# Optimization experiments

Measured on AMD Instinct MI355X. Metric: run time of the kernel, lower is better.

Reference implementation:

```python
import jax, jax.numpy as jnp
import numpy as np

B, H, W, C = 32, 112, 112, 128
R = 2048  # make_divisible(128*16, 8)

def setup_inputs() -> dict:
    key = jax.random.key(0)
    k1, k2, k3 = jax.random.split(key, 3)
    x = jax.random.normal(k1, (B, H, W, C), dtype=jnp.float32)
    w1 = jax.random.normal(k2, (C, R), dtype=jnp.float32) * (1.0 / np.sqrt(C))
    b1 = jnp.zeros((R,), dtype=jnp.float32)
    w2 = jax.random.normal(k3, (R, C), dtype=jnp.float32) * (1.0 / np.sqrt(R))
    b2 = jnp.zeros((C,), dtype=jnp.float32)
    return {"x": x, "w1": w1, "b1": b1, "w2": w2, "b2": b2}

def reference(x, w1, b1, w2, b2):
    # squeeze: global average pool over H, W -> [B, C]
    s = jnp.mean(x, axis=(1, 2))
    # excite: two 1x1 convs on pooled vector == matmuls
    h = jax.nn.gelu(s @ w1 + b1)          # [B, R], tanh-approx GELU (tfa default)
    g = jax.nn.sigmoid(h @ w2 + b2)       # [B, C]
    # broadcast gate over spatial dims
    return x * g[:, None, None, :]
```

## Files before the change

### kernel.cpp

```cpp
#include <hip/hip_runtime.h>
#include <math.h>

#define B_ 32
#define H_ 112
#define W_ 112
#define C_ 128
#define R_ 2048
#define HW_ (H_ * W_)
#define C4_ (C_ / 4)
#define PB_ 32
#define RB_ 8

typedef float f32x4_t __attribute__((ext_vector_type(4)));

__global__ __launch_bounds__(256) void pool_kernel(const float4* __restrict__ x,
                                                   float4* __restrict__ part) {
    const int b     = blockIdx.x;
    const int pb    = blockIdx.y;
    const int t     = threadIdx.x;
    const int lane4 = t & 31;
    const int prow  = t >> 5;

    const int pixels_per_block = HW_ / PB_;
    const int p0 = pb * pixels_per_block;
    const float4* xb = x + (size_t)b * HW_ * C4_;

    float4 acc = make_float4(0.f, 0.f, 0.f, 0.f);
    for (int p = p0 + prow; p < p0 + pixels_per_block; p += 8) {
        float4 v = xb[(size_t)p * C4_ + lane4];
        acc.x += v.x; acc.y += v.y; acc.z += v.z; acc.w += v.w;
    }

    __shared__ float4 red[256];
    red[t] = acc;
    __syncthreads();
    if (t < 32) {
        float4 a = red[t];
#pragma unroll
        for (int k = 1; k < 8; ++k) {
            float4 v = red[t + 32 * k];
            a.x += v.x; a.y += v.y; a.z += v.z; a.w += v.w;
        }
        part[((size_t)b * PB_ + pb) * C4_ + t] = a;
    }
}

__global__ __launch_bounds__(256) void fc_kernel(const float4* __restrict__ part,
                                                 const float* __restrict__ w1,
                                                 const float* __restrict__ b1,
                                                 const float4* __restrict__ w2,
                                                 float4* __restrict__ gpart) {
    const int b  = blockIdx.x >> 3;
    const int rb = blockIdx.x & 7;
    const int t  = threadIdx.x;
    const int r  = rb * 256 + t;

    __shared__ float  sl[C_];
    __shared__ float  hl[256];
    __shared__ float4 red[256];

    if (t < 32) {
        float4 a = make_float4(0.f, 0.f, 0.f, 0.f);
#pragma unroll 8
        for (int k = 0; k < PB_; ++k) {
            float4 v = part[((size_t)b * PB_ + k) * C4_ + t];
            a.x += v.x; a.y += v.y; a.z += v.z; a.w += v.w;
        }
        const float inv = 1.0f / (float)HW_;
        sl[t * 4 + 0] = a.x * inv;
        sl[t * 4 + 1] = a.y * inv;
        sl[t * 4 + 2] = a.z * inv;
        sl[t * 4 + 3] = a.w * inv;
    }
    __syncthreads();

    float acc = b1[r];
#pragma unroll 8
    for (int c = 0; c < C_; ++c)
        acc += sl[c] * w1[(size_t)c * R_ + r];

    const float xv = acc;
    const float tn = tanhf(0.7978845608028654f * (xv + 0.044715f * xv * xv * xv));
    hl[t] = 0.5f * xv * (1.0f + tn);
    __syncthreads();

    const int c4 = t & 31;
    const int ks = t >> 5;
    float4 a2 = make_float4(0.f, 0.f, 0.f, 0.f);
    const int rr0 = ks * 32;
#pragma unroll 8
    for (int rr = rr0; rr < rr0 + 32; ++rr) {
        const float hv = hl[rr];
        float4 w = w2[(size_t)(rb * 256 + rr) * C4_ + c4];
        a2.x += hv * w.x; a2.y += hv * w.y; a2.z += hv * w.z; a2.w += hv * w.w;
    }
    red[t] = a2;
    __syncthreads();
    if (t < 32) {
        float4 a = red[t];
#pragma unroll
        for (int k = 1; k < 8; ++k) {
            float4 v = red[t + 32 * k];
            a.x += v.x; a.y += v.y; a.z += v.z; a.w += v.w;
        }
        gpart[((size_t)b * RB_ + rb) * C4_ + t] = a;
    }
}

__global__ __launch_bounds__(256) void scale_kernel(const float4* __restrict__ x,
                                                    const float4* __restrict__ gpart,
                                                    const float* __restrict__ b2,
                                                    float4* __restrict__ out) {
    const int b  = blockIdx.x;
    const int t  = threadIdx.x;
    const int c4 = t & 31;

    const float4* gp = gpart + (size_t)b * RB_ * C4_;
    float4 a = gp[c4];
#pragma unroll
    for (int k = 1; k < RB_; ++k) {
        float4 v = gp[(size_t)k * C4_ + c4];
        a.x += v.x; a.y += v.y; a.z += v.z; a.w += v.w;
    }
    a.x += b2[c4 * 4 + 0]; a.y += b2[c4 * 4 + 1];
    a.z += b2[c4 * 4 + 2]; a.w += b2[c4 * 4 + 3];
    float4 gv;
    gv.x = 1.0f / (1.0f + expf(-a.x));
    gv.y = 1.0f / (1.0f + expf(-a.y));
    gv.z = 1.0f / (1.0f + expf(-a.z));
    gv.w = 1.0f / (1.0f + expf(-a.w));

    const size_t base = (size_t)b * HW_ * C4_;
    const int total = HW_ * C4_;
    const int stride = gridDim.y * 256;

    for (int i = blockIdx.y * 256 + t; i < total; i += stride) {
        float4 v = x[base + i];
        f32x4_t o;
        o.x = v.x * gv.x; o.y = v.y * gv.y; o.z = v.z * gv.z; o.w = v.w * gv.w;
        __builtin_nontemporal_store(o, (f32x4_t*)&out[base + i]);
    }
}

extern "C" void kernel_launch(void* const* d_in, const int* in_sizes, int n_in,
                              void* d_out, int out_size, void* d_ws, size_t ws_size,
                              hipStream_t stream) {
    const float* x  = (const float*)d_in[0];
    const float* w1 = (const float*)d_in[1];
    const float* b1 = (const float*)d_in[2];
    const float* w2 = (const float*)d_in[3];
    const float* b2 = (const float*)d_in[4];
    float* out = (float*)d_out;

    float* part  = (float*)d_ws;
    float* gpart = part + B_ * PB_ * C_;

    pool_kernel<<<dim3(B_, PB_), 256, 0, stream>>>((const float4*)x, (float4*)part);
    fc_kernel<<<B_ * RB_, 256, 0, stream>>>((const float4*)part, w1, b1,
                                            (const float4*)w2, (float4*)gpart);
    scale_kernel<<<dim3(B_, 64), 256, 0, stream>>>((const float4*)x,
                                                   (const float4*)gpart, b2,
                                                   (float4*)out);
}
```

Measured before the change: 393.4 us.

## Fuse pool, FC and scale into one cooperative kernel with grid syncs

Replaces the three launches with a single cooperative kernel that pools, computes the gate MLP, and scales, separated by two grid-wide syncs. Each block scales the same pixel slice it pooled, so the second read of x may hit the last-level cache, and launch overhead drops. It falls back to the original three kernels during stream capture or if the cooperative launch fails. The cost is grid-sync latency, plus the requirement that all 1024 blocks be co-resident.

```diff
diff --git a/kernel.cpp b/kernel.cpp
--- a/kernel.cpp
+++ b/kernel.cpp
@@ -1,5 +1,8 @@
 #include <hip/hip_runtime.h>
+#include <hip/hip_cooperative_groups.h>
 #include <math.h>
+
+namespace cg = cooperative_groups;
 
 #define B_ 32
 #define H_ 112
@@ -10,8 +13,137 @@
 #define C4_ (C_ / 4)
 #define PB_ 32
 #define RB_ 8
+#define NB_ (B_ * PB_)
 
 typedef float f32x4_t __attribute__((ext_vector_type(4)));
+
+__global__ __launch_bounds__(256, 4) void fused_kernel(
+    const float4* __restrict__ x, const float* __restrict__ w1,
+    const float* __restrict__ b1, const float4* __restrict__ w2,
+    const float* __restrict__ b2, float4* __restrict__ part,
+    float4* __restrict__ gpart, float4* __restrict__ out)
+{
+    cg::grid_group grid = cg::this_grid();
+    const int blk = blockIdx.x;
+    const int t   = threadIdx.x;
+
+    __shared__ float4 red[256];
+    __shared__ float  sl[C_];
+    __shared__ float  hl[256];
+
+    {
+        const int b     = blk >> 5;
+        const int pb    = blk & 31;
+        const int lane4 = t & 31;
+        const int prow  = t >> 5;
+        const int ppb   = HW_ / PB_;
+        const int p0    = pb * ppb;
+        const float4* xb = x + (size_t)b * HW_ * C4_;
+
+        float4 acc = make_float4(0.f, 0.f, 0.f, 0.f);
+        for (int p = p0 + prow; p < p0 + ppb; p += 8) {
+            float4 v = xb[(size_t)p * C4_ + lane4];
+            acc.x += v.x; acc.y += v.y; acc.z += v.z; acc.w += v.w;
+        }
+        red[t] = acc;
+        __syncthreads();
+        if (t < 32) {
+            float4 a = red[t];
+#pragma unroll
+            for (int k = 1; k < 8; ++k) {
+                float4 v = red[t + 32 * k];
+                a.x += v.x; a.y += v.y; a.z += v.z; a.w += v.w;
+            }
+            part[((size_t)b * PB_ + pb) * C4_ + t] = a;
+        }
+    }
+    grid.sync();
+
+    if (blk < B_ * RB_) {
+        const int b  = blk >> 3;
+        const int rb = blk & 7;
+        const int r  = rb * 256 + t;
+
+        if (t < 32) {
+            float4 a = make_float4(0.f, 0.f, 0.f, 0.f);
+#pragma unroll 8
+            for (int k = 0; k < PB_; ++k) {
+                float4 v = part[((size_t)b * PB_ + k) * C4_ + t];
+                a.x += v.x; a.y += v.y; a.z += v.z; a.w += v.w;
+            }
+            const float inv = 1.0f / (float)HW_;
+            sl[t * 4 + 0] = a.x * inv;
+            sl[t * 4 + 1] = a.y * inv;
+            sl[t * 4 + 2] = a.z * inv;
+            sl[t * 4 + 3] = a.w * inv;
+        }
+        __syncthreads();
+
+        float acc = b1[r];
+#pragma unroll 8
+        for (int c = 0; c < C_; ++c)
+            acc += sl[c] * w1[(size_t)c * R_ + r];
+
+        const float xv = acc;
+        const float tn = tanhf(0.7978845608028654f * (xv + 0.044715f * xv * xv * xv));
+        hl[t] = 0.5f * xv * (1.0f + tn);
+        __syncthreads();
+
+        const int c4 = t & 31;
+        const int ks = t >> 5;
+        float4 a2 = make_float4(0.f, 0.f, 0.f, 0.f);
+        const int rr0 = ks * 32;
+#pragma unroll 8
+        for (int rr = rr0; rr < rr0 + 32; ++rr) {
+            const float hv = hl[rr];
+            float4 w = w2[(size_t)(rb * 256 + rr) * C4_ + c4];
+            a2.x += hv * w.x; a2.y += hv * w.y; a2.z += hv * w.z; a2.w += hv * w.w;
+        }
+        red[t] = a2;
+        __syncthreads();
+        if (t < 32) {
+            float4 a = red[t];
+#pragma unroll
+            for (int k = 1; k < 8; ++k) {
+                float4 v = red[t + 32 * k];
+                a.x += v.x; a.y += v.y; a.z += v.z; a.w += v.w;
+            }
+            gpart[((size_t)b * RB_ + rb) * C4_ + t] = a;
+        }
+    }
+    grid.sync();
+
+    {
+        const int b  = blk >> 5;
+        const int pb = blk & 31;
+        const int c4 = t & 31;
+
+        const float4* gp = gpart + (size_t)b * RB_ * C4_;
+        float4 a = gp[c4];
+#pragma unroll
+        for (int k = 1; k < RB_; ++k) {
+            float4 v = gp[(size_t)k * C4_ + c4];
+            a.x += v.x; a.y += v.y; a.z += v.z; a.w += v.w;
+        }
+        a.x += b2[c4 * 4 + 0]; a.y += b2[c4 * 4 + 1];
+        a.z += b2[c4 * 4 + 2]; a.w += b2[c4 * 4 + 3];
+        float4 gv;
+        gv.x = 1.0f / (1.0f + expf(-a.x));
+        gv.y = 1.0f / (1.0f + expf(-a.y));
+        gv.z = 1.0f / (1.0f + expf(-a.z));
+        gv.w = 1.0f / (1.0f + expf(-a.w));
+
+        const int ppb = HW_ / PB_;
+        const size_t base = (size_t)b * HW_ * C4_ + (size_t)pb * ppb * C4_;
+        const int n = ppb * C4_;
+        for (int i = t; i < n; i += 256) {
+            float4 v = x[base + i];
+            f32x4_t o;
+            o.x = v.x * gv.x; o.y = v.y * gv.y; o.z = v.z * gv.z; o.w = v.w * gv.w;
+            __builtin_nontemporal_store(o, (f32x4_t*)&out[base + i]);
+        }
+    }
+}
 
 __global__ __launch_bounds__(256) void pool_kernel(const float4* __restrict__ x,
                                                    float4* __restrict__ part) {
@@ -145,20 +277,31 @@
 extern "C" void kernel_launch(void* const* d_in, const int* in_sizes, int n_in,
                               void* d_out, int out_size, void* d_ws, size_t ws_size,
                               hipStream_t stream) {
-    const float* x  = (const float*)d_in[0];
-    const float* w1 = (const float*)d_in[1];
-    const float* b1 = (const float*)d_in[2];
-    const float* w2 = (const float*)d_in[3];
-    const float* b2 = (const float*)d_in[4];
-    float* out = (float*)d_out;
-
-    float* part  = (float*)d_ws;
-    float* gpart = part + B_ * PB_ * C_;
-
-    pool_kernel<<<dim3(B_, PB_), 256, 0, stream>>>((const float4*)x, (float4*)part);
-    fc_kernel<<<B_ * RB_, 256, 0, stream>>>((const float4*)part, w1, b1,
-                                            (const float4*)w2, (float4*)gpart);
-    scale_kernel<<<dim3(B_, 64), 256, 0, stream>>>((const float4*)x,
-                                                   (const float4*)gpart, b2,
-                                                   (float4*)out);
-}
+    const float4* x  = (const float4*)d_in[0];
+    const float*  w1 = (const float*)d_in[1];
+    const float*  b1 = (const float*)d_in[2];
+    const float4* w2 = (const float4*)d_in[3];
+    const float*  b2 = (const float*)d_in[4];
+    float4* out = (float4*)d_out;
+
+    float4* part  = (float4*)d_ws;
+    float4* gpart = (float4*)((float*)d_ws + B_ * PB_ * C_);
+
+    hipStreamCaptureStatus cap = hipStreamCaptureStatusNone;
+    unsigned long long cap_id = 0;
+    (void)hipStreamGetCaptureInfo(stream, &cap, &cap_id);
+
+    if (cap == hipStreamCaptureStatusNone) {
+        void* args[] = {(void*)&x, (void*)&w1, (void*)&b1, (void*)&w2,
+                        (void*)&b2, (void*)&part, (void*)&gpart, (void*)&out};
+        hipError_t err = hipLaunchCooperativeKernel((void*)fused_kernel,
+                                                    dim3(NB_), dim3(256),
+                                                    args, 0, stream);
+        if (err == hipSuccess) return;
+        (void)hipGetLastError();
+    }
+
+    pool_kernel<<<dim3(B_, PB_), 256, 0, stream>>>(x, part);
+    fc_kernel<<<B_ * RB_, 256, 0, stream>>>(part, w1, b1, w2, gpart);
+    scale_kernel<<<dim3(B_, 64), 256, 0, stream>>>(x, gpart, (const float*)b2, out);
+}
```

After: 392.7 us. About the same (-0.2%).
